# Kernel tuning notes

Measured on AMD Instinct MI355X. Metric: run time of the kernel, lower is better.

The kernel has to match this reference:

```python
import jax, jax.numpy as jnp
import numpy as np
from jax import lax

SUB_NO = 20; T_NO = 200; BASIS_NO = 19; T_DATA = 100000; E_NO = 800; I_NO = 200


def make_cos_basis():
    # raised-cosine log-time basis, [BASIS_NO, T_NO]
    i = jnp.arange(BASIS_NO, dtype=jnp.float32)[:, None]
    phi = (jnp.pi / 2.0) * i
    x = jnp.arange(T_NO, dtype=jnp.float32)[None, :]
    raw = 5.0 * jnp.log(x + 1.0)  # cos_scale=5, cos_shift=1
    basis = 0.5 * jnp.cos(raw - phi) + 0.5
    return jnp.where((raw >= phi - jnp.pi) & (raw <= phi + jnp.pi), basis, 0.0)


def causal_group_conv(x, kern):
    # x: [T, sub], kern: [sub, T_no]; out[t,k] = sum_j kern[k,j]*x[t-j,k]
    xr = x.T[None]  # [1, sub, T]
    w = jnp.flip(kern, 1)[:, None, :]  # [sub, 1, T_no]
    out = lax.conv_general_dilated(xr, w, (1,), [(T_NO - 1, 0)],
                                   dimension_numbers=('NCH', 'OIH', 'NCH'),
                                   feature_group_count=kern.shape[0])
    return out[0].T  # [T, sub]


def hist_conv(z, kern):
    # matches torch: pad T_no leading zeros, valid corr with flipped kernel, drop last
    zp = jnp.concatenate([jnp.zeros((T_NO,), z.dtype), z])[None, None, :]
    w = jnp.flip(kern)[None, None, :]
    out = lax.conv_general_dilated(zp, w, (1,), 'VALID',
                                   dimension_numbers=('NCH', 'OIH', 'NCH'))
    return out[0, 0, :-1]  # [T]


def setup_inputs() -> dict:
    key = jax.random.key(0)
    ks = jax.random.split(key, 12)
    # binary dendritic tree: parent of node j is (j-1)//2; C_den[p, j] = 1
    parent = np.maximum((np.arange(SUB_NO) - 1) // 2, 0)
    C_den = np.zeros((SUB_NO, SUB_NO), np.float32)
    for j in range(1, SUB_NO):
        C_den[parent[j], j] = 1.0
    assign_e = jax.random.randint(ks[0], (E_NO,), 0, SUB_NO)
    assign_i = jax.random.randint(ks[1], (I_NO,), 0, SUB_NO)
    C_syn_e = jax.nn.one_hot(assign_e, SUB_NO, dtype=jnp.float32).T
    C_syn_i = jax.nn.one_hot(assign_i, SUB_NO, dtype=jnp.float32).T
    S_e = (jax.random.uniform(ks[2], (T_DATA, E_NO)) < 0.05).astype(jnp.float32)
    S_i = (jax.random.uniform(ks[3], (T_DATA, I_NO)) < 0.05).astype(jnp.float32)
    Z = (jax.random.uniform(ks[4], (T_DATA,)) < 0.02).astype(jnp.float32)
    return {
        'S_e': S_e, 'S_i': S_i, 'Z': Z,
        'C_den': jnp.asarray(C_den), 'C_syn_e': C_syn_e, 'C_syn_i': C_syn_i,
        'W_syn_ns': 0.1 * jax.random.normal(ks[5], (SUB_NO, BASIS_NO, 2)),
        'W_syn_s': 0.1 * jax.random.normal(ks[6], (SUB_NO, BASIS_NO, 2)),
        'W_sub_ns': 0.1 * jnp.ones((SUB_NO,), jnp.float32),
        'W_sub_s': 0.1 * jnp.ones((SUB_NO,), jnp.float32),
        'V_o': jax.random.normal(ks[7], (1,)),
        'Theta_ns': 0.1 * jax.random.normal(ks[8], (SUB_NO,)),
        'Theta_s': 0.1 * jax.random.normal(ks[9], (SUB_NO,)),
        'hist_s_weights': 0.1 * jax.random.normal(ks[10], (BASIS_NO,)),
        'hist_ns_weights': 0.1 * jax.random.normal(ks[11], (BASIS_NO,)),
    }


def reference(S_e, S_i, Z, C_den, C_syn_e, C_syn_i, W_syn_ns, W_syn_s,
              W_sub_ns, W_sub_s, V_o, Theta_ns, Theta_s,
              hist_s_weights, hist_ns_weights):
    cb = make_cos_basis()
    syn_e = S_e @ C_syn_e.T  # [T, sub]
    syn_i = S_i @ C_syn_i.T
    e_kern_ns = W_syn_ns[:, :, 0] @ cb  # [sub, T_no]
    i_kern_ns = W_syn_ns[:, :, 1] @ cb
    e_kern_s = W_syn_s[:, :, 0] @ cb
    i_kern_s = W_syn_s[:, :, 1] @ cb
    syn_ns = causal_group_conv(syn_e, e_kern_ns) + causal_group_conv(syn_i, i_kern_ns)
    syn_s = causal_group_conv(syn_e, e_kern_s) + causal_group_conv(syn_i, i_kern_s)
    ws2 = W_sub_s ** 2
    wns2 = W_sub_ns ** 2
    T = S_e.shape[0]
    s_out = jnp.zeros((T, SUB_NO), syn_s.dtype)
    ns_out = jnp.zeros((T, SUB_NO), syn_ns.dtype)
    # leaf-to-root tree message passing; C_den[k] masks children of node k
    for k in range(SUB_NO - 1, 0, -1):
        mask = C_den[k]
        s_out = s_out.at[:, k].set(jnp.tanh(syn_s[:, k] + s_out @ (mask * ws2) + Theta_s[k]))
        ns_out = ns_out.at[:, k].set(jnp.tanh(syn_ns[:, k] + ns_out @ (mask * wns2) + Theta_ns[k]))
    hist_s_kern = hist_s_weights @ cb  # [T_no]
    hist_ns_kern = hist_ns_weights @ cb
    root_mask = C_den[0]
    final_Z = jax.nn.sigmoid(hist_conv(Z, hist_s_kern) + syn_s[:, 0]
                             + s_out @ (root_mask * ws2) + Theta_s[0])
    root_ns = jnp.tanh(hist_conv(Z, hist_ns_kern) + syn_ns[:, 0]
                       + ns_out @ (root_mask * wns2) + Theta_ns[0])
    final_V = root_ns * wns2[0] + V_o[0]
    out_filters = jnp.vstack([e_kern_ns, i_kern_ns, e_kern_s, i_kern_s,
                              hist_ns_kern[None], hist_s_kern[None]])
    return final_V, final_Z, out_filters
```

## Files before the change

kernel.cpp:

```cpp
#include <hip/hip_runtime.h>
#include <hip/hip_bf16.h>
#include <math.h>

#define SUB_NO 20
#define T_NO   200
#define BASIS_NO 19
#define T_DATA 100000
#define E_NO   800
#define I_NO   200

using u16 = unsigned short;
using u32 = unsigned int;
using u64 = unsigned long long;

__device__ __forceinline__ float bf2f(u16 h) {
  return __builtin_bit_cast(float, (u32)h << 16);
}
__device__ __forceinline__ u16 f2bf(float f) {
  u32 u = __builtin_bit_cast(u32, f);
  u += 0x7FFFu + ((u >> 16) & 1u);
  return (u16)(u >> 16);
}
__device__ __forceinline__ float ldx(const void* p, int i, bool bf) {
  return bf ? bf2f(((const u16*)p)[i]) : ((const float*)p)[i];
}
__device__ __forceinline__ void stx(void* p, int i, float v, bool bf) {
  if (bf) ((u16*)p)[i] = f2bf(v); else ((float*)p)[i] = v;
}

#define K0_BLOCKS 21
__global__ __launch_bounds__(256) void k0_prep(
    const u32* __restrict__ probe,
    const void* __restrict__ Wns, const void* __restrict__ Ws,
    const void* __restrict__ hsw, const void* __restrict__ hnsw,
    const void* __restrict__ Cse, const void* __restrict__ Csi,
    float* __restrict__ kern4, float* __restrict__ hist_s,
    float* __restrict__ hist_ns, int* __restrict__ ae, int* __restrict__ ai,
    void* __restrict__ out) {
  const bool bf = (probe[0] != 0u);
  __shared__ float cb[BASIS_NO * T_NO];
  const int tid = threadIdx.x;
  constexpr float PI = 3.14159265358979323846f;
  for (int idx = tid; idx < BASIS_NO * T_NO; idx += 256) {
    int b = idx / T_NO, j = idx - b * T_NO;
    float phi = 0.5f * PI * (float)b;
    float raw = 5.0f * logf((float)j + 1.0f);
    float v = 0.f;
    if (raw >= phi - PI && raw <= phi + PI) v = 0.5f * cosf(raw - phi) + 0.5f;
    cb[idx] = v;
  }
  __syncthreads();
  const int fbase = 2 * T_DATA;
  for (int gid = blockIdx.x * 256 + tid; gid < 5200; gid += K0_BLOCKS * 256) {
    if (gid < 4000) {
      int k = gid / T_NO, j = gid - k * T_NO;
      float e_ns = 0.f, i_ns = 0.f, e_s = 0.f, i_s = 0.f;
#pragma unroll
      for (int b = 0; b < BASIS_NO; ++b) {
        float c = cb[b * T_NO + j];
        e_ns = fmaf(ldx(Wns, (k * BASIS_NO + b) * 2 + 0, bf), c, e_ns);
        i_ns = fmaf(ldx(Wns, (k * BASIS_NO + b) * 2 + 1, bf), c, i_ns);
        e_s  = fmaf(ldx(Ws,  (k * BASIS_NO + b) * 2 + 0, bf), c, e_s);
        i_s  = fmaf(ldx(Ws,  (k * BASIS_NO + b) * 2 + 1, bf), c, i_s);
      }
      float* kp = kern4 + (j * SUB_NO + k) * 4;
      kp[0] = e_ns; kp[1] = e_s; kp[2] = i_ns; kp[3] = i_s;
      stx(out, fbase + (0 * SUB_NO + k) * T_NO + j, e_ns, bf);
      stx(out, fbase + (1 * SUB_NO + k) * T_NO + j, i_ns, bf);
      stx(out, fbase + (2 * SUB_NO + k) * T_NO + j, e_s,  bf);
      stx(out, fbase + (3 * SUB_NO + k) * T_NO + j, i_s,  bf);
    } else if (gid < 4200) {
      int j = gid - 4000;
      float hs = 0.f, hns = 0.f;
#pragma unroll
      for (int b = 0; b < BASIS_NO; ++b) {
        float c = cb[b * T_NO + j];
        hs  = fmaf(ldx(hsw,  b, bf), c, hs);
        hns = fmaf(ldx(hnsw, b, bf), c, hns);
      }
      hist_s[j] = hs; hist_ns[j] = hns;
      stx(out, fbase + 80 * T_NO + j, hns, bf);
      stx(out, fbase + 81 * T_NO + j, hs,  bf);
    } else if (gid < 5000) {
      int e = gid - 4200;
      int a = 0;
      for (int k = 0; k < SUB_NO; ++k) if (ldx(Cse, k * E_NO + e, bf) != 0.f) a = k;
      ae[e] = a;
    } else {
      int e = gid - 5000;
      int a = 0;
      for (int k = 0; k < SUB_NO; ++k) if (ldx(Csi, k * I_NO + e, bf) != 0.f) a = k;
      ai[e] = a;
    }
  }
}

#define K1_R 64

__global__ __launch_bounds__(256) void k1_agg(
    const u32* __restrict__ probe,
    const void* __restrict__ Se, const void* __restrict__ Si,
    const int* __restrict__ ae, const int* __restrict__ ai,
    u32* __restrict__ syn_pair) {
  const bool bf = (probe[0] != 0u);
  __shared__ u64 mask_e[SUB_NO][16];
  __shared__ u64 mask_i[SUB_NO][8];
  __shared__ int lae[E_NO];
  __shared__ int lai[I_NO];
  const int tid = threadIdx.x;
  const int l = tid & 63;
  const int wv = tid >> 6;
  for (int n = tid; n < E_NO; n += 256) lae[n] = ae[n];
  for (int n = tid; n < I_NO; n += 256) lai[n] = ai[n];
  __syncthreads();
  for (int pid = tid; pid < 480; pid += 256) {
    if (pid < 320) {
      int k = pid >> 4, w = pid & 15;
      u64 m = 0;
      if (bf) {
        if (w < 8) { for (int b = 0; b < 64; ++b) if (lae[8 * b + w] == k) m |= 1ull << b; }
        else       { for (int b = 0; b < 36; ++b) if (lae[512 + 8 * b + (w - 8)] == k) m |= 1ull << b; }
      } else {
        int g = w >> 2, j = w & 3;
        int lim = (g < 3) ? 64 : 8;
        for (int b = 0; b < lim; ++b) if (lae[256 * g + 4 * b + j] == k) m |= 1ull << b;
      }
      mask_e[k][w] = m;
    } else {
      int p2 = pid - 320; int k = p2 >> 3, w = p2 & 7;
      u64 m = 0;
      if (bf) { for (int b = 0; b < 25; ++b) { int e = 8 * b + w; if (e < I_NO && lai[e] == k) m |= 1ull << b; } }
      else if (w < 4) { for (int b = 0; b < 50; ++b) if (lai[4 * b + w] == k) m |= 1ull << b; }
      mask_i[k][w] = m;
    }
  }
  __syncthreads();
  u64 rme[16], rmi[8];
  const int ke = (l < SUB_NO) ? l : 0;
  const int ki = (l >= 32 && l < 32 + SUB_NO) ? l - 32 : 0;
#pragma unroll
  for (int w = 0; w < 16; ++w) rme[w] = mask_e[ke][w];
#pragma unroll
  for (int w = 0; w < 8; ++w) rmi[w] = mask_i[ki][w];

  const int r0 = blockIdx.x * K1_R + wv * 16;
  int nrows = T_DATA - r0; if (nrows > 16) nrows = 16;
  if (nrows <= 0) return;
  const uint4 z4 = make_uint4(0u, 0u, 0u, 0u);

  if (bf) {
    uint4 a0, a1, c0;
    {
      const uint4* p = (const uint4*)((const u16*)Se + (size_t)r0 * E_NO);
      a0 = p[l]; a1 = (l < 36) ? p[64 + l] : z4;
      const uint4* pi = (const uint4*)((const u16*)Si + (size_t)r0 * I_NO);
      c0 = (l < 25) ? pi[l] : z4;
    }
    for (int i = 0; i < nrows; ++i) {
      const int t = r0 + i;
      uint4 b0 = z4, b1 = z4, d0 = z4;
      if (i + 1 < nrows) {
        const uint4* p = (const uint4*)((const u16*)Se + (size_t)(t + 1) * E_NO);
        b0 = p[l]; b1 = (l < 36) ? p[64 + l] : z4;
        const uint4* pi = (const uint4*)((const u16*)Si + (size_t)(t + 1) * I_NO);
        d0 = (l < 25) ? pi[l] : z4;
      }
      u32 ce = 0, ci = 0;
#pragma unroll
      for (int j = 0; j < 8; ++j) {
        u32 d = (&a0.x)[j >> 1];
        u32 h = (j & 1) ? (d >> 16) : (d & 0xFFFFu);
        u64 m = __ballot(h != 0u);
        ce += (u32)__popcll(rme[j] & m);
      }
#pragma unroll
      for (int j = 0; j < 8; ++j) {
        u32 d = (&a1.x)[j >> 1];
        u32 h = (j & 1) ? (d >> 16) : (d & 0xFFFFu);
        u64 m = __ballot(h != 0u);
        ce += (u32)__popcll(rme[8 + j] & m);
      }
#pragma unroll
      for (int j = 0; j < 8; ++j) {
        u32 d = (&c0.x)[j >> 1];
        u32 h = (j & 1) ? (d >> 16) : (d & 0xFFFFu);
        u64 m = __ballot(h != 0u);
        ci += (u32)__popcll(rmi[j] & m);
      }
      u32 pe = (u32)f2bf((float)ce);
      u32 pif = (u32)f2bf((float)ci);
      u32 other = __shfl(pif, (l + 32) & 63, 64);
      if (l < SUB_NO) syn_pair[(size_t)t * SUB_NO + l] = pe | (other << 16);
      a0 = b0; a1 = b1; c0 = d0;
    }
  } else {
    uint4 a0, a1, a2, a3, c0;
    {
      const uint4* p = (const uint4*)((const float*)Se + (size_t)r0 * E_NO);
      a0 = p[l]; a1 = p[64 + l]; a2 = p[128 + l]; a3 = (l < 8) ? p[192 + l] : z4;
      const uint4* pi = (const uint4*)((const float*)Si + (size_t)r0 * I_NO);
      c0 = (l < 50) ? pi[l] : z4;
    }
    for (int i = 0; i < nrows; ++i) {
      const int t = r0 + i;
      uint4 b0 = z4, b1 = z4, b2 = z4, b3 = z4, d0 = z4;
      if (i + 1 < nrows) {
        const uint4* p = (const uint4*)((const float*)Se + (size_t)(t + 1) * E_NO);
        b0 = p[l]; b1 = p[64 + l]; b2 = p[128 + l]; b3 = (l < 8) ? p[192 + l] : z4;
        const uint4* pi = (const uint4*)((const float*)Si + (size_t)(t + 1) * I_NO);
        d0 = (l < 50) ? pi[l] : z4;
      }
      u32 ce = 0, ci = 0;
      const uint4 va[4] = {a0, a1, a2, a3};
#pragma unroll
      for (int g = 0; g < 4; ++g) {
#pragma unroll
        for (int j = 0; j < 4; ++j) {
          u32 d = (&va[g].x)[j];
          u64 m = __ballot(d != 0u);
          ce += (u32)__popcll(rme[4 * g + j] & m);
        }
      }
#pragma unroll
      for (int j = 0; j < 4; ++j) {
        u32 d = (&c0.x)[j];
        u64 m = __ballot(d != 0u);
        ci += (u32)__popcll(rmi[j] & m);
      }
      u32 pe = (u32)f2bf((float)ce);
      u32 pif = (u32)f2bf((float)ci);
      u32 other = __shfl(pif, (l + 32) & 63, 64);
      if (l < SUB_NO) syn_pair[(size_t)t * SUB_NO + l] = pe | (other << 16);
      a0 = b0; a1 = b1; a2 = b2; a3 = b3; c0 = d0;
    }
  }
}

#define K2T  128
#define K2R  (K2T + T_NO)
#define K2CH 20

__global__ __launch_bounds__(320, 5) void k2_conv(
    const u32* __restrict__ probe,
    const u32* __restrict__ syn_pair, const float* __restrict__ kern4,
    const float* __restrict__ hist_s, const float* __restrict__ hist_ns,
    const void* __restrict__ Z, const void* __restrict__ Wsub_ns,
    const void* __restrict__ Wsub_s, const void* __restrict__ Vo,
    const void* __restrict__ Thns, const void* __restrict__ Ths,
    void* __restrict__ out) {
  const bool bf = (probe[0] != 0u);
  __shared__ __align__(16) unsigned char smem[K2R * SUB_NO * 4];
  uint4* tile4 = (uint4*)smem;
  float* accsh = (float*)smem;
  float* hp    = (float*)(smem + 21000);
  __shared__ float4 kc4[K2CH * SUB_NO];
  __shared__ float ztile[K2R];
  __shared__ float lhs[T_NO], lhns[T_NO];
  __shared__ float ws2_l[SUB_NO], wns2_l[SUB_NO], ths_l[SUB_NO], thns_l[SUB_NO];
  const int tid = threadIdx.x;
  const int l = tid & 63;
  const int kg = tid >> 6;
  const int t0 = blockIdx.x * K2T;

  const int base4 = (t0 - T_NO) * (SUB_NO / 4);
  const uint4* sp4 = (const uint4*)syn_pair;
  for (int n = tid; n < K2R * 5; n += 320) {
    int g = base4 + n;
    uint4 v = make_uint4(0u, 0u, 0u, 0u);
    if (g >= 0 && g < T_DATA * SUB_NO / 4) v = sp4[g];
    tile4[n] = v;
  }
  const int zbase = t0 - T_NO;
  for (int n = tid; n < K2R; n += 320) {
    int g = zbase + n;
    ztile[n] = (g >= 0 && g < T_DATA) ? ldx(Z, g, bf) : 0.f;
  }
  for (int n = tid; n < T_NO; n += 320) { lhs[n] = hist_s[n]; lhns[n] = hist_ns[n]; }
  if (tid < SUB_NO) {
    float w = ldx(Wsub_s, tid, bf);   ws2_l[tid]  = w * w;
    float wn = ldx(Wsub_ns, tid, bf); wns2_l[tid] = wn * wn;
    ths_l[tid]  = ldx(Ths, tid, bf);
    thns_l[tid] = ldx(Thns, tid, bf);
  }
  __syncthreads();

  float2 acc_a[4], acc_b[4];
#pragma unroll
  for (int j = 0; j < 4; ++j) {
    acc_a[j] = make_float2(0.f, 0.f);
    acc_b[j] = make_float2(0.f, 0.f);
  }
  float hs_a = 0.f, hns_a = 0.f, hs_b = 0.f, hns_b = 0.f;
  const int mlo = 40 * kg;

  for (int ch = 0; ch < T_NO / K2CH; ++ch) {
    const float4* ksrc = (const float4*)(kern4 + ch * K2CH * SUB_NO * 4);
    for (int n = tid; n < K2CH * SUB_NO; n += 320) kc4[n] = ksrc[n];
    __syncthreads();
#pragma unroll 2
    for (int mm = 0; mm < K2CH; ++mm) {
      const int m = ch * K2CH + mm;
      uint4 qa = tile4[(l + T_NO - m) * 5 + kg];
      uint4 qb = tile4[(l + 64 + T_NO - m) * 5 + kg];
      if ((unsigned)(m - mlo) < 40u) {
        float ls = lhs[m], lns = lhns[m];
        float za = ztile[l + T_NO - 1 - m];
        float zb = ztile[l + 64 + T_NO - 1 - m];
        hs_a = fmaf(ls, za, hs_a);   hns_a = fmaf(lns, za, hns_a);
        hs_b = fmaf(ls, zb, hs_b);   hns_b = fmaf(lns, zb, hns_b);
      }
      const float4* kp = &kc4[mm * SUB_NO + kg * 4];
#pragma unroll
      for (int j = 0; j < 4; ++j) {
        float4 c = kp[j];
        u32 ua = (&qa.x)[j], ub = (&qb.x)[j];
        float ea = __builtin_bit_cast(float, ua << 16);
        float ia = __builtin_bit_cast(float, ua & 0xFFFF0000u);
        float eb = __builtin_bit_cast(float, ub << 16);
        float ib = __builtin_bit_cast(float, ub & 0xFFFF0000u);
        acc_a[j].x = fmaf(c.x, ea, acc_a[j].x);
        acc_a[j].y = fmaf(c.y, ea, acc_a[j].y);
        acc_a[j].x = fmaf(c.z, ia, acc_a[j].x);
        acc_a[j].y = fmaf(c.w, ia, acc_a[j].y);
        acc_b[j].x = fmaf(c.x, eb, acc_b[j].x);
        acc_b[j].y = fmaf(c.y, eb, acc_b[j].y);
        acc_b[j].x = fmaf(c.z, ib, acc_b[j].x);
        acc_b[j].y = fmaf(c.w, ib, acc_b[j].y);
      }
    }
    __syncthreads();
  }

#pragma unroll
  for (int j = 0; j < 4; ++j) {
    const int k = kg * 4 + j;
    accsh[l * 41 + k]            = acc_a[j].y;
    accsh[l * 41 + 20 + k]       = acc_a[j].x;
    accsh[(l + 64) * 41 + k]      = acc_b[j].y;
    accsh[(l + 64) * 41 + 20 + k] = acc_b[j].x;
  }
  float* hp_s = hp;
  float* hp_ns = hp + 640;
  hp_s[kg * 128 + l] = hs_a;  hp_s[kg * 128 + 64 + l] = hs_b;
  hp_ns[kg * 128 + l] = hns_a; hp_ns[kg * 128 + 64 + l] = hns_b;
  __syncthreads();

  if (kg < 2) {
    const int tl = kg * 64 + l;
    float h_s = 0.f, h_ns = 0.f;
#pragma unroll
    for (int w = 0; w < 5; ++w) { h_s += hp_s[w * 128 + tl]; h_ns += hp_ns[w * 128 + tl]; }
    const float* ar = &accsh[tl * 41];
    float so[SUB_NO], no[SUB_NO];
#pragma unroll
    for (int k = SUB_NO - 1; k >= 1; --k) {
      float as_ = ar[k] + ths_l[k];
      float an_ = ar[20 + k] + thns_l[k];
      const int c1 = 2 * k + 1, c2 = 2 * k + 2;
      if (c1 < SUB_NO) { as_ += ws2_l[c1] * so[c1]; an_ += wns2_l[c1] * no[c1]; }
      if (c2 < SUB_NO) { as_ += ws2_l[c2] * so[c2]; an_ += wns2_l[c2] * no[c2]; }
      so[k] = tanhf(as_);
      no[k] = tanhf(an_);
    }
    float zs = h_s + ar[0] + ths_l[0] + ws2_l[1] * so[1] + ws2_l[2] * so[2];
    float zn = h_ns + ar[20] + thns_l[0] + wns2_l[1] * no[1] + wns2_l[2] * no[2];
    float fZ = 1.f / (1.f + expf(-zs));
    float fV = tanhf(zn) * wns2_l[0] + ldx(Vo, 0, bf);
    const int t = t0 + tl;
    if (t < T_DATA) {
      stx(out, t, fV, bf);
      stx(out, T_DATA + t, fZ, bf);
    }
  }
}

extern "C" void kernel_launch(void* const* d_in, const int* in_sizes, int n_in,
                              void* d_out, int out_size, void* d_ws, size_t ws_size,
                              hipStream_t stream) {
  const void* Se      = d_in[0];
  const void* Si      = d_in[1];
  const void* Z       = d_in[2];
  const u32*  probe   = (const u32*)d_in[3];
  const void* Cse     = d_in[4];
  const void* Csi     = d_in[5];
  const void* Wns     = d_in[6];
  const void* Ws_     = d_in[7];
  const void* Wsub_ns = d_in[8];
  const void* Wsub_s  = d_in[9];
  const void* Vo      = d_in[10];
  const void* Thns    = d_in[11];
  const void* Ths     = d_in[12];
  const void* hsw     = d_in[13];
  const void* hnsw    = d_in[14];

  float* wsf      = (float*)d_ws;
  float* kern4    = wsf;
  float* hist_s   = wsf + 16000;
  float* hist_ns  = wsf + 16200;
  int*   ae       = (int*)(wsf + 16400);
  int*   ai       = (int*)(wsf + 17200);
  u32*   syn_pair = (u32*)(wsf + 17408);

  hipLaunchKernelGGL(k0_prep, dim3(K0_BLOCKS), dim3(256), 0, stream,
                     probe, Wns, Ws_, hsw, hnsw, Cse, Csi,
                     kern4, hist_s, hist_ns, ae, ai, d_out);
  hipLaunchKernelGGL(k1_agg, dim3((T_DATA + K1_R - 1) / K1_R), dim3(256), 0, stream,
                     probe, Se, Si, ae, ai, syn_pair);
  hipLaunchKernelGGL(k2_conv, dim3((T_DATA + K2T - 1) / K2T), dim3(320), 0, stream,
                     probe, syn_pair, kern4, hist_s, hist_ns, Z,
                     Wsub_ns, Wsub_s, Vo, Thns, Ths, d_out);
}
```

Before: 648.8 us.

## Read conv taps via uniform scalar loads and unroll spike aggregation by two rows

```diff
diff --git a/kernel.cpp b/kernel.cpp
--- a/kernel.cpp
+++ b/kernel.cpp
@@ -97,7 +97,50 @@
 
 #define K1_R 64
 
-__global__ __launch_bounds__(256) void k1_agg(
+__device__ __forceinline__ void k1_load_bf(const void* Se, const void* Si,
+                                           int t, int l, uint4& a0, uint4& a1,
+                                           uint4& c0) {
+  const uint4 z4 = make_uint4(0u, 0u, 0u, 0u);
+  const uint4* p = (const uint4*)((const u16*)Se + (size_t)t * E_NO);
+  a0 = p[l]; a1 = (l < 36) ? p[64 + l] : z4;
+  const uint4* pi = (const uint4*)((const u16*)Si + (size_t)t * I_NO);
+  c0 = (l < 25) ? pi[l] : z4;
+}
+
+__device__ __forceinline__ void k1_proc_bf(uint4 a0, uint4 a1, uint4 c0,
+                                           const u64* rme, const u64* rmi,
+                                           int l, int t,
+                                           u32* __restrict__ syn_pair) {
+  u32 ce = 0, ci = 0;
+#pragma unroll
+  for (int j = 0; j < 8; ++j) {
+    u32 d = (&a0.x)[j >> 1];
+    u32 h = (j & 1) ? (d >> 16) : (d & 0xFFFFu);
+    u64 m = __ballot(h != 0u);
+    ce += (u32)__popcll(rme[j] & m);
+  }
+#pragma unroll
+  for (int j = 0; j < 8; ++j) {
+    u32 d = (&a1.x)[j >> 1];
+    u32 h = (j & 1) ? (d >> 16) : (d & 0xFFFFu);
+    u64 m = __ballot(h != 0u);
+    ce += (u32)__popcll(rme[8 + j] & m);
+  }
+#pragma unroll
+  for (int j = 0; j < 8; ++j) {
+    u32 d = (&c0.x)[j >> 1];
+    u32 h = (j & 1) ? (d >> 16) : (d & 0xFFFFu);
+    u64 m = __ballot(h != 0u);
+    ci += (u32)__popcll(rmi[j] & m);
+  }
+  if (l < SUB_NO) {
+    u32 pe = (u32)f2bf((float)ce);
+    u32 pif = (u32)f2bf((float)ci);
+    syn_pair[(size_t)t * SUB_NO + l] = pe | (pif << 16);
+  }
+}
+
+__global__ __launch_bounds__(256, 4) void k1_agg(
     const u32* __restrict__ probe,
     const void* __restrict__ Se, const void* __restrict__ Si,
     const int* __restrict__ ae, const int* __restrict__ ai,
@@ -136,62 +179,30 @@
   }
   __syncthreads();
   u64 rme[16], rmi[8];
-  const int ke = (l < SUB_NO) ? l : 0;
-  const int ki = (l >= 32 && l < 32 + SUB_NO) ? l - 32 : 0;
-#pragma unroll
-  for (int w = 0; w < 16; ++w) rme[w] = mask_e[ke][w];
-#pragma unroll
-  for (int w = 0; w < 8; ++w) rmi[w] = mask_i[ki][w];
+  const int kk = (l < SUB_NO) ? l : 0;
+#pragma unroll
+  for (int w = 0; w < 16; ++w) rme[w] = mask_e[kk][w];
+#pragma unroll
+  for (int w = 0; w < 8; ++w) rmi[w] = mask_i[kk][w];
 
   const int r0 = blockIdx.x * K1_R + wv * 16;
-  int nrows = T_DATA - r0; if (nrows > 16) nrows = 16;
-  if (nrows <= 0) return;
+  if (r0 >= T_DATA) return;
   const uint4 z4 = make_uint4(0u, 0u, 0u, 0u);
 
   if (bf) {
-    uint4 a0, a1, c0;
-    {
-      const uint4* p = (const uint4*)((const u16*)Se + (size_t)r0 * E_NO);
-      a0 = p[l]; a1 = (l < 36) ? p[64 + l] : z4;
-      const uint4* pi = (const uint4*)((const u16*)Si + (size_t)r0 * I_NO);
-      c0 = (l < 25) ? pi[l] : z4;
-    }
-    for (int i = 0; i < nrows; ++i) {
-      const int t = r0 + i;
-      uint4 b0 = z4, b1 = z4, d0 = z4;
-      if (i + 1 < nrows) {
-        const uint4* p = (const uint4*)((const u16*)Se + (size_t)(t + 1) * E_NO);
-        b0 = p[l]; b1 = (l < 36) ? p[64 + l] : z4;
-        const uint4* pi = (const uint4*)((const u16*)Si + (size_t)(t + 1) * I_NO);
-        d0 = (l < 25) ? pi[l] : z4;
-      }
-      u32 ce = 0, ci = 0;
-#pragma unroll
-      for (int j = 0; j < 8; ++j) {
-        u32 d = (&a0.x)[j >> 1];
-        u32 h = (j & 1) ? (d >> 16) : (d & 0xFFFFu);
-        u64 m = __ballot(h != 0u);
-        ce += (u32)__popcll(rme[j] & m);
-      }
-#pragma unroll
-      for (int j = 0; j < 8; ++j) {
-        u32 d = (&a1.x)[j >> 1];
-        u32 h = (j & 1) ? (d >> 16) : (d & 0xFFFFu);
-        u64 m = __ballot(h != 0u);
-        ce += (u32)__popcll(rme[8 + j] & m);
-      }
-#pragma unroll
-      for (int j = 0; j < 8; ++j) {
-        u32 d = (&c0.x)[j >> 1];
-        u32 h = (j & 1) ? (d >> 16) : (d & 0xFFFFu);
-        u64 m = __ballot(h != 0u);
-        ci += (u32)__popcll(rmi[j] & m);
-      }
-      u32 pe = (u32)f2bf((float)ce);
-      u32 pif = (u32)f2bf((float)ci);
-      u32 other = __shfl(pif, (l + 32) & 63, 64);
-      if (l < SUB_NO) syn_pair[(size_t)t * SUB_NO + l] = pe | (other << 16);
-      a0 = b0; a1 = b1; c0 = d0;
+    uint4 A0, A1, C0, B0, B1, D0;
+    k1_load_bf(Se, Si, r0, l, A0, A1, C0);
+    k1_load_bf(Se, Si, r0 + 1, l, B0, B1, D0);
+    for (int i = 0; i < 16; i += 2) {
+      uint4 N0 = z4, N1 = z4, M0 = z4, M1 = z4, P0 = z4, Q0 = z4;
+      if (i + 2 < 16) {
+        k1_load_bf(Se, Si, r0 + i + 2, l, N0, N1, P0);
+        k1_load_bf(Se, Si, r0 + i + 3, l, M0, M1, Q0);
+      }
+      k1_proc_bf(A0, A1, C0, rme, rmi, l, r0 + i, syn_pair);
+      k1_proc_bf(B0, B1, D0, rme, rmi, l, r0 + i + 1, syn_pair);
+      A0 = N0; A1 = N1; C0 = P0;
+      B0 = M0; B1 = M1; D0 = Q0;
     }
   } else {
     uint4 a0, a1, a2, a3, c0;
@@ -201,10 +212,10 @@
       const uint4* pi = (const uint4*)((const float*)Si + (size_t)r0 * I_NO);
       c0 = (l < 50) ? pi[l] : z4;
     }
-    for (int i = 0; i < nrows; ++i) {
+    for (int i = 0; i < 16; ++i) {
       const int t = r0 + i;
       uint4 b0 = z4, b1 = z4, b2 = z4, b3 = z4, d0 = z4;
-      if (i + 1 < nrows) {
+      if (i + 1 < 16) {
         const uint4* p = (const uint4*)((const float*)Se + (size_t)(t + 1) * E_NO);
         b0 = p[l]; b1 = p[64 + l]; b2 = p[128 + l]; b3 = (l < 8) ? p[192 + l] : z4;
         const uint4* pi = (const uint4*)((const float*)Si + (size_t)(t + 1) * I_NO);
@@ -227,10 +238,11 @@
         u64 m = __ballot(d != 0u);
         ci += (u32)__popcll(rmi[j] & m);
       }
-      u32 pe = (u32)f2bf((float)ce);
-      u32 pif = (u32)f2bf((float)ci);
-      u32 other = __shfl(pif, (l + 32) & 63, 64);
-      if (l < SUB_NO) syn_pair[(size_t)t * SUB_NO + l] = pe | (other << 16);
+      if (l < SUB_NO) {
+        u32 pe = (u32)f2bf((float)ce);
+        u32 pif = (u32)f2bf((float)ci);
+        syn_pair[(size_t)t * SUB_NO + l] = pe | (pif << 16);
+      }
       a0 = b0; a1 = b1; a2 = b2; a3 = b3; c0 = d0;
     }
   }
@@ -238,9 +250,8 @@
 
 #define K2T  128
 #define K2R  (K2T + T_NO)
-#define K2CH 20
-
-__global__ __launch_bounds__(320, 5) void k2_conv(
+
+__global__ __launch_bounds__(320, 6) void k2_conv(
     const u32* __restrict__ probe,
     const u32* __restrict__ syn_pair, const float* __restrict__ kern4,
     const float* __restrict__ hist_s, const float* __restrict__ hist_ns,
@@ -253,13 +264,12 @@
   uint4* tile4 = (uint4*)smem;
   float* accsh = (float*)smem;
   float* hp    = (float*)(smem + 21000);
-  __shared__ float4 kc4[K2CH * SUB_NO];
   __shared__ float ztile[K2R];
   __shared__ float lhs[T_NO], lhns[T_NO];
   __shared__ float ws2_l[SUB_NO], wns2_l[SUB_NO], ths_l[SUB_NO], thns_l[SUB_NO];
   const int tid = threadIdx.x;
   const int l = tid & 63;
-  const int kg = tid >> 6;
+  const int kgu = __builtin_amdgcn_readfirstlane(tid >> 6);
   const int t0 = blockIdx.x * K2T;
 
   const int base4 = (t0 - T_NO) * (SUB_NO / 4);
@@ -291,62 +301,61 @@
     acc_b[j] = make_float2(0.f, 0.f);
   }
   float hs_a = 0.f, hns_a = 0.f, hs_b = 0.f, hns_b = 0.f;
-  const int mlo = 40 * kg;
-
-  for (int ch = 0; ch < T_NO / K2CH; ++ch) {
-    const float4* ksrc = (const float4*)(kern4 + ch * K2CH * SUB_NO * 4);
-    for (int n = tid; n < K2CH * SUB_NO; n += 320) kc4[n] = ksrc[n];
-    __syncthreads();
+  const int mlo = 40 * kgu;
+  const float4* kb = (const float4*)kern4 + kgu * 4;
+
 #pragma unroll 2
-    for (int mm = 0; mm < K2CH; ++mm) {
-      const int m = ch * K2CH + mm;
-      uint4 qa = tile4[(l + T_NO - m) * 5 + kg];
-      uint4 qb = tile4[(l + 64 + T_NO - m) * 5 + kg];
-      if ((unsigned)(m - mlo) < 40u) {
-        float ls = lhs[m], lns = lhns[m];
-        float za = ztile[l + T_NO - 1 - m];
-        float zb = ztile[l + 64 + T_NO - 1 - m];
-        hs_a = fmaf(ls, za, hs_a);   hns_a = fmaf(lns, za, hns_a);
-        hs_b = fmaf(ls, zb, hs_b);   hns_b = fmaf(lns, zb, hns_b);
-      }
-      const float4* kp = &kc4[mm * SUB_NO + kg * 4];
-#pragma unroll
-      for (int j = 0; j < 4; ++j) {
-        float4 c = kp[j];
-        u32 ua = (&qa.x)[j], ub = (&qb.x)[j];
-        float ea = __builtin_bit_cast(float, ua << 16);
-        float ia = __builtin_bit_cast(float, ua & 0xFFFF0000u);
-        float eb = __builtin_bit_cast(float, ub << 16);
-        float ib = __builtin_bit_cast(float, ub & 0xFFFF0000u);
-        acc_a[j].x = fmaf(c.x, ea, acc_a[j].x);
-        acc_a[j].y = fmaf(c.y, ea, acc_a[j].y);
-        acc_a[j].x = fmaf(c.z, ia, acc_a[j].x);
-        acc_a[j].y = fmaf(c.w, ia, acc_a[j].y);
-        acc_b[j].x = fmaf(c.x, eb, acc_b[j].x);
-        acc_b[j].y = fmaf(c.y, eb, acc_b[j].y);
-        acc_b[j].x = fmaf(c.z, ib, acc_b[j].x);
-        acc_b[j].y = fmaf(c.w, ib, acc_b[j].y);
-      }
-    }
-    __syncthreads();
-  }
+  for (int m = 0; m < T_NO; ++m) {
+    float4 c0 = kb[m * 5 * 4 + 0];
+    float4 c1 = kb[m * 5 * 4 + 1];
+    float4 c2 = kb[m * 5 * 4 + 2];
+    float4 c3 = kb[m * 5 * 4 + 3];
+    uint4 qa = tile4[(l + T_NO - m) * 5 + kgu];
+    uint4 qb = tile4[(l + 64 + T_NO - m) * 5 + kgu];
+    if ((unsigned)(m - mlo) < 40u) {
+      float ls = lhs[m], lns = lhns[m];
+      float za = ztile[l + T_NO - 1 - m];
+      float zb = ztile[l + 64 + T_NO - 1 - m];
+      hs_a = fmaf(ls, za, hs_a);   hns_a = fmaf(lns, za, hns_a);
+      hs_b = fmaf(ls, zb, hs_b);   hns_b = fmaf(lns, zb, hns_b);
+    }
+    const float4 cc[4] = {c0, c1, c2, c3};
+#pragma unroll
+    for (int j = 0; j < 4; ++j) {
+      float4 c = cc[j];
+      u32 ua = (&qa.x)[j], ub = (&qb.x)[j];
+      float ea = __builtin_bit_cast(float, ua << 16);
+      float ia = __builtin_bit_cast(float, ua & 0xFFFF0000u);
+      float eb = __builtin_bit_cast(float, ub << 16);
+      float ib = __builtin_bit_cast(float, ub & 0xFFFF0000u);
+      acc_a[j].x = fmaf(c.x, ea, acc_a[j].x);
+      acc_a[j].y = fmaf(c.y, ea, acc_a[j].y);
+      acc_a[j].x = fmaf(c.z, ia, acc_a[j].x);
+      acc_a[j].y = fmaf(c.w, ia, acc_a[j].y);
+      acc_b[j].x = fmaf(c.x, eb, acc_b[j].x);
+      acc_b[j].y = fmaf(c.y, eb, acc_b[j].y);
+      acc_b[j].x = fmaf(c.z, ib, acc_b[j].x);
+      acc_b[j].y = fmaf(c.w, ib, acc_b[j].y);
+    }
+  }
+  __syncthreads();
 
 #pragma unroll
   for (int j = 0; j < 4; ++j) {
-    const int k = kg * 4 + j;
-    accsh[l * 41 + k]            = acc_a[j].y;
-    accsh[l * 41 + 20 + k]       = acc_a[j].x;
+    const int k = kgu * 4 + j;
+    accsh[l * 41 + k]             = acc_a[j].y;
+    accsh[l * 41 + 20 + k]        = acc_a[j].x;
     accsh[(l + 64) * 41 + k]      = acc_b[j].y;
     accsh[(l + 64) * 41 + 20 + k] = acc_b[j].x;
   }
   float* hp_s = hp;
   float* hp_ns = hp + 640;
-  hp_s[kg * 128 + l] = hs_a;  hp_s[kg * 128 + 64 + l] = hs_b;
-  hp_ns[kg * 128 + l] = hns_a; hp_ns[kg * 128 + 64 + l] = hns_b;
-  __syncthreads();
-
-  if (kg < 2) {
-    const int tl = kg * 64 + l;
+  hp_s[kgu * 128 + l] = hs_a;   hp_s[kgu * 128 + 64 + l] = hs_b;
+  hp_ns[kgu * 128 + l] = hns_a; hp_ns[kgu * 128 + 64 + l] = hns_b;
+  __syncthreads();
+
+  if (kgu < 2) {
+    const int tl = kgu * 64 + l;
     float h_s = 0.f, h_ns = 0.f;
 #pragma unroll
     for (int w = 0; w < 5; ++w) { h_s += hp_s[w * 128 + tl]; h_ns += hp_ns[w * 128 + tl]; }
```

Result: faster. 617.7 us (-4.8%).
